# Kernel tuning notes

Hardware: AMD Instinct MI355X
Metric: run time of the kernel (lower is better)

Reference implementation:

```python
import jax, jax.numpy as jnp
import numpy as np

N, E = 50000, 640000          # nodes, edges
F_IN, HID, CLS = 128, 128, 64  # feature dims


def setup_inputs() -> dict:
    key = jax.random.key(0)
    ks = jax.random.split(key, 12)
    x = jax.random.normal(ks[0], (N, F_IN), dtype=jnp.float32)
    edge_index = jax.random.randint(ks[1], (2, E), 0, N, dtype=jnp.int32)
    s_in = 1.0 / np.sqrt(F_IN)
    s_h = 1.0 / np.sqrt(HID)
    return {
        "x": x,
        "edge_index": edge_index,
        "W0": jax.random.normal(ks[2], (F_IN, HID), jnp.float32) * s_in,
        "b0": jnp.zeros((HID,), jnp.float32),
        "W1": jax.random.normal(ks[3], (HID, HID), jnp.float32) * s_h,
        "b1": jnp.zeros((HID,), jnp.float32),
        "W2": jax.random.normal(ks[4], (HID, HID), jnp.float32) * s_h,
        "b2": jnp.zeros((HID,), jnp.float32),
        "W_lin": jax.random.normal(ks[5], (HID, CLS), jnp.float32) * s_h,
        "b_lin": jnp.zeros((CLS,), jnp.float32),
    }


def reference(x, edge_index, W0, b0, W1, b1, W2, b2, W_lin, b_lin):
    # GCNConv (PyG defaults): out = D^-1/2 (A + I) D^-1/2 (x @ W) + b
    row, col = edge_index[0], edge_index[1]  # source -> target
    # degree with self-loop (graph is fixed across layers, compute norms once)
    deg = jnp.zeros((N,), x.dtype).at[col].add(1.0) + 1.0
    dinv = jax.lax.rsqrt(deg)                 # deg >= 1, safe
    enorm = (dinv[row] * dinv[col])[:, None]  # [E,1] edge norm
    snorm = (dinv * dinv)[:, None]            # [N,1] self-loop norm

    def conv(h, W, b):
        h = h @ W                                             # [N,HID]
        agg = jnp.zeros_like(h).at[col].add(h[row] * enorm)   # neighbor agg
        return agg + h * snorm + b                            # + self loop + bias

    h = jax.nn.relu(conv(x, W0, b0))
    h = jax.nn.relu(conv(h, W1, b1))
    h = jax.nn.relu(conv(h, W2, b2))
    return h @ W_lin + b_lin
```

## Files before the change

kernel.cpp:

```cpp
#include <hip/hip_runtime.h>
#include <hip/hip_fp16.h>

#define N_NODES 50000
#define HID 128
#define CLS 64

#define NBINS 196
#define NBLK 256
#define LBUF_CAP 4096
#define WTOT 57344
#define GEMM0_BLOCKS 782
#define AROW 136

typedef __attribute__((ext_vector_type(8))) _Float16 f16x8;
typedef __attribute__((ext_vector_type(4))) float f32x4;

__device__ __forceinline__ float2 u2f2(unsigned int u) {
    union { unsigned int u; __half2 h; } c;
    c.u = u;
    return __half22float2(c.h);
}
__device__ __forceinline__ unsigned int f2u2(float a, float b) {
    union { unsigned int u; __half2 h; } c;
    c.h = __float22half2_rn(make_float2(a, b));
    return c.u;
}

__global__ __launch_bounds__(256) void hist_wsplit_kernel(
    const int* __restrict__ col, int* __restrict__ hist,
    const float* __restrict__ W0, const float* __restrict__ W1,
    const float* __restrict__ W2, const float* __restrict__ Wl,
    __half* __restrict__ o0h, __half* __restrict__ o0l,
    __half* __restrict__ o1h, __half* __restrict__ o1l,
    __half* __restrict__ o2h, __half* __restrict__ o2l,
    __half* __restrict__ o3h, __half* __restrict__ o3l,
    int E, int chunk) {
    int widx = blockIdx.x * 256 + threadIdx.x;
    if (widx < WTOT) {
        const float* W;
        __half *oh, *ol;
        int NCdim, local;
        if (widx < 16384)      { W = W0; oh = o0h; ol = o0l; NCdim = 128; local = widx; }
        else if (widx < 32768) { W = W1; oh = o1h; ol = o1l; NCdim = 128; local = widx - 16384; }
        else if (widx < 49152) { W = W2; oh = o2h; ol = o2l; NCdim = 128; local = widx - 32768; }
        else                   { W = Wl; oh = o3h; ol = o3l; NCdim = 64;  local = widx - 49152; }
        int nn = local >> 7;
        int k = local & 127;
        float v = W[(size_t)k * NCdim + nn];
        __half h = __float2half_rn(v);
        oh[local] = h;
        ol[local] = __float2half_rn(v - __half2float(h));
    }
    __shared__ int h[NBINS];
    for (int i = threadIdx.x; i < NBINS; i += 256) h[i] = 0;
    __syncthreads();
    int b = blockIdx.x;
    int beg = b * chunk;
    int end = min(E, beg + chunk);
    if (beg < end) {
        int vend = beg + ((end - beg) & ~3);
        for (int i = beg + threadIdx.x * 4; i < vend; i += 1024) {
            int4 c4 = *(const int4*)(col + i);
            atomicAdd(&h[c4.x >> 8], 1);
            atomicAdd(&h[c4.y >> 8], 1);
            atomicAdd(&h[c4.z >> 8], 1);
            atomicAdd(&h[c4.w >> 8], 1);
        }
        int i = vend + threadIdx.x;
        if (i < end) atomicAdd(&h[col[i] >> 8], 1);
    }
    __syncthreads();
    for (int i = threadIdx.x; i < NBINS; i += 256)
        hist[i * NBLK + b] = h[i];
}

__global__ __launch_bounds__(256) void scatter_kernel(
    const int* __restrict__ row, const int* __restrict__ col,
    const int* __restrict__ hist, int* __restrict__ binBase_g,
    int* __restrict__ sbuf_src, unsigned char* __restrict__ sbuf_c,
    int E, int chunk) {
    __shared__ int sTot[256];
    __shared__ int cur[NBINS];
    int b = blockIdx.x, t = threadIdx.x;
    int partial = 0, total = 0;
    if (t < NBINS) {
        const int4* r4 = (const int4*)(hist + t * NBLK);
        int nb4 = b >> 2, rem = b & 3;
        for (int j = 0; j < NBLK / 4; ++j) {
            int4 v = r4[j];
            int s = v.x + v.y + v.z + v.w;
            total += s;
            if (j < nb4) partial += s;
            else if (j == nb4) {
                if (rem > 0) partial += v.x;
                if (rem > 1) partial += v.y;
                if (rem > 2) partial += v.z;
            }
        }
    }
    sTot[t] = (t < NBINS) ? total : 0;
    __syncthreads();
#pragma unroll
    for (int off = 1; off < 256; off <<= 1) {
        int u = (t >= off) ? sTot[t - off] : 0;
        __syncthreads();
        sTot[t] += u;
        __syncthreads();
    }
    int myBase = sTot[t] - total;
    if (t < NBINS) cur[t] = myBase + partial;
    if (b == 0) {
        if (t < NBINS) binBase_g[t] = myBase;
        if (t == 0) binBase_g[NBINS] = E;
    }
    __syncthreads();
    int beg = b * chunk;
    int end = min(E, beg + chunk);
    if (beg >= end) return;
    int vend = beg + ((end - beg) & ~3);
    for (int i = beg + t * 4; i < vend; i += 1024) {
        int4 c4 = *(const int4*)(col + i);
        int4 r4 = *(const int4*)(row + i);
        int p;
        p = atomicAdd(&cur[c4.x >> 8], 1); sbuf_src[p] = r4.x; sbuf_c[p] = (unsigned char)(c4.x & 255);
        p = atomicAdd(&cur[c4.y >> 8], 1); sbuf_src[p] = r4.y; sbuf_c[p] = (unsigned char)(c4.y & 255);
        p = atomicAdd(&cur[c4.z >> 8], 1); sbuf_src[p] = r4.z; sbuf_c[p] = (unsigned char)(c4.z & 255);
        p = atomicAdd(&cur[c4.w >> 8], 1); sbuf_src[p] = r4.w; sbuf_c[p] = (unsigned char)(c4.w & 255);
    }
    int i = vend + t;
    if (i < end) {
        int c = col[i];
        int p = atomicAdd(&cur[c >> 8], 1);
        sbuf_src[p] = row[i];
        sbuf_c[p] = (unsigned char)(c & 255);
    }
}

__device__ __forceinline__ void gemm0_body(
    const float* __restrict__ x, const __half* __restrict__ Bh,
    const __half* __restrict__ Bl, __half* __restrict__ C, int M, int rowTile) {
    constexpr int NT = 8;
    int lane = threadIdx.x & 63;
    int m0 = rowTile << 4;
    if (m0 >= M) return;
    int mr = lane & 15;
    int kq = (lane >> 4) << 3;

    const float*  af = x + (size_t)(m0 + mr) * 128 + kq;
    const __half* bh = Bh + (size_t)mr * 128 + kq;
    const __half* bl = Bl + (size_t)mr * 128 + kq;

    f32x4 acc[NT];
#pragma unroll
    for (int t = 0; t < NT; ++t) acc[t] = (f32x4){0.f, 0.f, 0.f, 0.f};
#pragma unroll
    for (int kc = 0; kc < 128; kc += 32) {
        float4 lo = *(const float4*)(af + kc);
        float4 hi = *(const float4*)(af + kc + 4);
        f16x8 a;
        a[0] = (_Float16)lo.x; a[1] = (_Float16)lo.y;
        a[2] = (_Float16)lo.z; a[3] = (_Float16)lo.w;
        a[4] = (_Float16)hi.x; a[5] = (_Float16)hi.y;
        a[6] = (_Float16)hi.z; a[7] = (_Float16)hi.w;
#pragma unroll
        for (int t = 0; t < NT; ++t) {
            f16x8 wh = *(const f16x8*)(bh + (size_t)t * 16 * 128 + kc);
            f16x8 wl = *(const f16x8*)(bl + (size_t)t * 16 * 128 + kc);
            acc[t] = __builtin_amdgcn_mfma_f32_16x16x32_f16(a, wh, acc[t], 0, 0, 0);
            acc[t] = __builtin_amdgcn_mfma_f32_16x16x32_f16(a, wl, acc[t], 0, 0, 0);
        }
    }
    int r0 = m0 + ((lane >> 4) << 2);
    int cc = lane & 15;
#pragma unroll
    for (int t = 0; t < NT; ++t)
#pragma unroll
        for (int r = 0; r < 4; ++r)
            C[(size_t)(r0 + r) * 128 + t * 16 + cc] =
                __float2half_rn(acc[t][r]);
}

__global__ __launch_bounds__(256) void csrplace_gemm0_kernel(
    const int* __restrict__ binBase,
    const int* __restrict__ sbuf_src, const unsigned char* __restrict__ sbuf_c,
    float* __restrict__ dinv, int* __restrict__ row_ptr, int* __restrict__ csr_src,
    const float* __restrict__ x, const __half* __restrict__ W0h,
    const __half* __restrict__ W0l, __half* __restrict__ h2, int n, int E) {
    __shared__ int lcnt[256];
    __shared__ int lcur[256];
    __shared__ int ss[256];
    __shared__ int lbuf[LBUF_CAP];
    int b = blockIdx.x;
    if (b >= NBINS) {
        gemm0_body(x, W0h, W0l, h2, n, (b - NBINS) * 4 + (threadIdx.x >> 6));
        return;
    }
    int t = threadIdx.x;
    lcnt[t] = 0;
    __syncthreads();
    int beg = binBase[b], end = binBase[b + 1];
    for (int j = beg + t; j < end; j += 256)
        atomicAdd(&lcnt[sbuf_c[j]], 1);
    __syncthreads();
    int deg = lcnt[t];
    int node = b * 256 + t;
    if (node < n) dinv[node] = rsqrtf((float)deg + 1.0f);
    ss[t] = deg;
    __syncthreads();
#pragma unroll
    for (int off = 1; off < 256; off <<= 1) {
        int u = (t >= off) ? ss[t - off] : 0;
        __syncthreads();
        ss[t] += u;
        __syncthreads();
    }
    int excl = ss[t] - deg;
    lcur[t] = excl;
    int total = ss[255];
    if (node < n) row_ptr[node] = beg + excl;
    if (b == 0 && t == 0) row_ptr[n] = E;
    __syncthreads();
    for (int j = beg + t; j < end; j += 256) {
        int c = sbuf_c[j];
        int pos = atomicAdd(&lcur[c], 1);
        lbuf[pos] = sbuf_src[j];
    }
    __syncthreads();
    for (int j = t; j < total; j += 256) csr_src[beg + j] = lbuf[j];
}

__device__ __forceinline__ void gather_batch(
    const __half* __restrict__ h2, int msrc, float mw, int cnt,
    int hw, int foff, float4& acc) {
    int pairs = (cnt + 1) >> 1;
    int j = 0;
    for (; j + 4 <= pairs; j += 4) {
        int i0 = (j << 1) + hw,       i1 = ((j + 1) << 1) + hw;
        int i2 = ((j + 2) << 1) + hw, i3 = ((j + 3) << 1) + hw;
        int s0 = __shfl(msrc, i0), s1 = __shfl(msrc, i1);
        int s2 = __shfl(msrc, i2), s3 = __shfl(msrc, i3);
        float w0 = __shfl(mw, i0), w1 = __shfl(mw, i1);
        float w2 = __shfl(mw, i2), w3 = __shfl(mw, i3);
        uint2 r0 = *(const uint2*)(h2 + ((size_t)s0 << 7) + foff);
        uint2 r1 = *(const uint2*)(h2 + ((size_t)s1 << 7) + foff);
        uint2 r2 = *(const uint2*)(h2 + ((size_t)s2 << 7) + foff);
        uint2 r3 = *(const uint2*)(h2 + ((size_t)s3 << 7) + foff);
        float2 a0 = u2f2(r0.x), b0 = u2f2(r0.y);
        float2 a1 = u2f2(r1.x), b1 = u2f2(r1.y);
        float2 a2 = u2f2(r2.x), b2 = u2f2(r2.y);
        float2 a3 = u2f2(r3.x), b3 = u2f2(r3.y);
        acc.x = fmaf(a0.x, w0, acc.x); acc.y = fmaf(a0.y, w0, acc.y);
        acc.z = fmaf(b0.x, w0, acc.z); acc.w = fmaf(b0.y, w0, acc.w);
        acc.x = fmaf(a1.x, w1, acc.x); acc.y = fmaf(a1.y, w1, acc.y);
        acc.z = fmaf(b1.x, w1, acc.z); acc.w = fmaf(b1.y, w1, acc.w);
        acc.x = fmaf(a2.x, w2, acc.x); acc.y = fmaf(a2.y, w2, acc.y);
        acc.z = fmaf(b2.x, w2, acc.z); acc.w = fmaf(b2.y, w2, acc.w);
        acc.x = fmaf(a3.x, w3, acc.x); acc.y = fmaf(a3.y, w3, acc.y);
        acc.z = fmaf(b3.x, w3, acc.z); acc.w = fmaf(b3.y, w3, acc.w);
    }
    for (; j < pairs; ++j) {
        int i0 = (j << 1) + hw;
        int s0 = __shfl(msrc, i0);
        float w0 = __shfl(mw, i0);
        uint2 r0 = *(const uint2*)(h2 + ((size_t)s0 << 7) + foff);
        float2 a0 = u2f2(r0.x), b0 = u2f2(r0.y);
        acc.x = fmaf(a0.x, w0, acc.x); acc.y = fmaf(a0.y, w0, acc.y);
        acc.z = fmaf(b0.x, w0, acc.z); acc.w = fmaf(b0.y, w0, acc.w);
    }
}

template<int NC, bool HEAD>
__global__ __launch_bounds__(256) void agg_gemm_kernel(
    const __half* __restrict__ h2, const int* __restrict__ row_ptr,
    const int* __restrict__ csr_src, const float* __restrict__ dinv,
    const float* __restrict__ bias,
    const __half* __restrict__ Bh, const __half* __restrict__ Bl,
    const float* __restrict__ gbias, void* __restrict__ Cv, int n) {
    __shared__ __align__(16) __half Als[16][AROW];
    int wave = threadIdx.x >> 6;
    int lane = threadIdx.x & 63;
    int hw = lane >> 5;
    int foff = (lane & 31) << 2;
    int m0 = blockIdx.x << 4;
    int wid_base = m0 + wave * 4;

    int beg4[4], end4[4];
    float dv4[4];
#pragma unroll
    for (int k = 0; k < 4; ++k) {
        beg4[k] = row_ptr[wid_base + k];
        end4[k] = row_ptr[wid_base + k + 1];
        dv4[k] = dinv[wid_base + k];
    }
    int msrc4[4];
#pragma unroll
    for (int k = 0; k < 4; ++k) {
        int cnt = min(64, end4[k] - beg4[k]);
        msrc4[k] = 0;
        if (lane < cnt) msrc4[k] = csr_src[beg4[k] + lane];
    }
    float mw4[4];
#pragma unroll
    for (int k = 0; k < 4; ++k) {
        int cnt = min(64, end4[k] - beg4[k]);
        mw4[k] = 0.f;
        if (lane < cnt) mw4[k] = dinv[msrc4[k]] * dv4[k];
    }

#pragma unroll
    for (int k = 0; k < 4; ++k) {
        int wid = wid_base + k;
        float dv = dv4[k];
        float4 acc = make_float4(0.f, 0.f, 0.f, 0.f);
        int cnt0 = min(64, end4[k] - beg4[k]);
        gather_batch(h2, msrc4[k], mw4[k], cnt0, hw, foff, acc);
        for (int base = beg4[k] + 64; base < end4[k]; base += 64) {
            int cnt = min(64, end4[k] - base);
            int msrc = 0;
            float mw = 0.f;
            if (lane < cnt) {
                msrc = csr_src[base + lane];
                mw = dinv[msrc] * dv;
            }
            gather_batch(h2, msrc, mw, cnt, hw, foff, acc);
        }
        acc.x += __shfl_xor(acc.x, 32);
        acc.y += __shfl_xor(acc.y, 32);
        acc.z += __shfl_xor(acc.z, 32);
        acc.w += __shfl_xor(acc.w, 32);
        float sn = dv * dv;
        uint2 sr = *(const uint2*)(h2 + ((size_t)wid << 7) + foff);
        float2 s01 = u2f2(sr.x), s23 = u2f2(sr.y);
        float4 b4 = *(const float4*)(bias + foff);
        float o0 = fmaxf(fmaf(s01.x, sn, acc.x) + b4.x, 0.f);
        float o1 = fmaxf(fmaf(s01.y, sn, acc.y) + b4.y, 0.f);
        float o2 = fmaxf(fmaf(s23.x, sn, acc.z) + b4.z, 0.f);
        float o3 = fmaxf(fmaf(s23.y, sn, acc.w) + b4.w, 0.f);
        if (hw == 0) {
            int lr = wave * 4 + k;
            *(uint2*)&Als[lr][foff] = make_uint2(f2u2(o0, o1), f2u2(o2, o3));
        }
    }
    __syncthreads();

    constexpr int NT = NC / 16;
    constexpr int TPW = NT / 4;
    int mr = lane & 15;
    int kq = (lane >> 4) << 3;
    const __half* bh = Bh + (size_t)mr * 128 + kq;
    const __half* bl = Bl + (size_t)mr * 128 + kq;

    f32x4 acc[TPW];
#pragma unroll
    for (int t = 0; t < TPW; ++t) acc[t] = (f32x4){0.f, 0.f, 0.f, 0.f};
#pragma unroll
    for (int kc = 0; kc < 128; kc += 32) {
        f16x8 a = *(const f16x8*)&Als[mr][kq + kc];
#pragma unroll
        for (int t = 0; t < TPW; ++t) {
            int tile = wave * TPW + t;
            f16x8 wh = *(const f16x8*)(bh + (size_t)tile * 16 * 128 + kc);
            f16x8 wl = *(const f16x8*)(bl + (size_t)tile * 16 * 128 + kc);
            acc[t] = __builtin_amdgcn_mfma_f32_16x16x32_f16(a, wh, acc[t], 0, 0, 0);
            acc[t] = __builtin_amdgcn_mfma_f32_16x16x32_f16(a, wl, acc[t], 0, 0, 0);
        }
    }
    int r0 = m0 + ((lane >> 4) << 2);
    int cc = lane & 15;
#pragma unroll
    for (int t = 0; t < TPW; ++t) {
        int tile = wave * TPW + t;
        float bsv = HEAD ? gbias[tile * 16 + cc] : 0.f;
#pragma unroll
        for (int r = 0; r < 4; ++r) {
            if (r0 + r >= n) break;
            size_t idx = (size_t)(r0 + r) * NC + tile * 16 + cc;
            float val = acc[t][r] + bsv;
            if (HEAD)
                ((float*)Cv)[idx] = val;
            else
                ((__half*)Cv)[idx] = __float2half_rn(val);
        }
    }
}

extern "C" void kernel_launch(void* const* d_in, const int* in_sizes, int n_in,
                              void* d_out, int out_size, void* d_ws, size_t ws_size,
                              hipStream_t stream) {
    const float* x  = (const float*)d_in[0];
    const int* ei   = (const int*)d_in[1];
    const float* W0 = (const float*)d_in[2];
    const float* b0 = (const float*)d_in[3];
    const float* W1 = (const float*)d_in[4];
    const float* b1 = (const float*)d_in[5];
    const float* W2 = (const float*)d_in[6];
    const float* b2 = (const float*)d_in[7];
    const float* Wl = (const float*)d_in[8];
    const float* bl = (const float*)d_in[9];
    float* out = (float*)d_out;

    const int N = N_NODES;
    const int E = in_sizes[1] / 2;
    const int* row = ei;
    const int* col = ei + E;
    const int chunk = (((E + NBLK - 1) / NBLK) + 3) & ~3;

    char* ws = (char*)d_ws;
    auto alloc = [&](size_t bytes) {
        char* p = ws;
        ws += (bytes + 255) & ~(size_t)255;
        return p;
    };
    int*   hist    = (int*)alloc((size_t)NBINS * NBLK * 4);
    int*   binBase = (int*)alloc((size_t)(NBINS + 1) * 4);
    int*   sbuf_src= (int*)alloc((size_t)E * 4);
    unsigned char* sbuf_c = (unsigned char*)alloc((size_t)E);
    int*   row_ptr = (int*)alloc((size_t)(N + 1) * 4);
    float* dinv    = (float*)alloc((size_t)N * 4);
    int*   csr_src = (int*)alloc((size_t)E * 4);
    __half* h2a    = (__half*)alloc((size_t)N * HID * 2);
    __half* h2b    = (__half*)alloc((size_t)N * HID * 2);
    __half* Wt_h[4];
    __half* Wt_l[4];
    for (int i = 0; i < 3; ++i) {
        Wt_h[i] = (__half*)alloc((size_t)HID * HID * 2);
        Wt_l[i] = (__half*)alloc((size_t)HID * HID * 2);
    }
    Wt_h[3] = (__half*)alloc((size_t)CLS * HID * 2);
    Wt_l[3] = (__half*)alloc((size_t)CLS * HID * 2);

    hist_wsplit_kernel<<<NBLK, 256, 0, stream>>>(col, hist, W0, W1, W2, Wl,
        Wt_h[0], Wt_l[0], Wt_h[1], Wt_l[1], Wt_h[2], Wt_l[2], Wt_h[3], Wt_l[3], E, chunk);
    scatter_kernel<<<NBLK, 256, 0, stream>>>(row, col, hist, binBase, sbuf_src, sbuf_c, E, chunk);
    csrplace_gemm0_kernel<<<NBINS + GEMM0_BLOCKS, 256, 0, stream>>>(
        binBase, sbuf_src, sbuf_c, dinv, row_ptr, csr_src,
        x, Wt_h[0], Wt_l[0], h2a, N, E);

    const int fusedBlocks = (N + 15) / 16;

    agg_gemm_kernel<128, false><<<fusedBlocks, 256, 0, stream>>>(
        h2a, row_ptr, csr_src, dinv, b0, Wt_h[1], Wt_l[1], nullptr, h2b, N);
    agg_gemm_kernel<128, false><<<fusedBlocks, 256, 0, stream>>>(
        h2b, row_ptr, csr_src, dinv, b1, Wt_h[2], Wt_l[2], nullptr, h2a, N);
    agg_gemm_kernel<64, true><<<fusedBlocks, 256, 0, stream>>>(
        h2a, row_ptr, csr_src, dinv, b2, Wt_h[3], Wt_l[3], bl, out, N);
}
```

Measured before the change: 287.5 us.

## Interleave neighbor gathers across four rows with full-wave per-row feature split

Each wave now gathers for its four destination nodes together, looping to the maximum degree and issuing one edge per row per step. Each lane loads a half2 covering two features, so the whole 64-lane wave spans one 128-wide row instead of half-waves each handling four features and being reduced by a cross-half shuffle. This aims to keep more independent memory loads in flight and remove the reduction. Rows with fewer neighbors run masked, zero-weight iterations up to the group maximum, and each load is narrower. The row bound check in the GEMM store was also dropped, relying on N being a multiple of 16.

```diff
diff --git a/kernel.cpp b/kernel.cpp
--- a/kernel.cpp
+++ b/kernel.cpp
@@ -14,17 +14,6 @@
 
 typedef __attribute__((ext_vector_type(8))) _Float16 f16x8;
 typedef __attribute__((ext_vector_type(4))) float f32x4;
-
-__device__ __forceinline__ float2 u2f2(unsigned int u) {
-    union { unsigned int u; __half2 h; } c;
-    c.u = u;
-    return __half22float2(c.h);
-}
-__device__ __forceinline__ unsigned int f2u2(float a, float b) {
-    union { unsigned int u; __half2 h; } c;
-    c.h = __float22half2_rn(make_float2(a, b));
-    return c.u;
-}
 
 __global__ __launch_bounds__(256) void hist_wsplit_kernel(
     const int* __restrict__ col, int* __restrict__ hist,
@@ -229,46 +218,6 @@
     for (int j = t; j < total; j += 256) csr_src[beg + j] = lbuf[j];
 }
 
-__device__ __forceinline__ void gather_batch(
-    const __half* __restrict__ h2, int msrc, float mw, int cnt,
-    int hw, int foff, float4& acc) {
-    int pairs = (cnt + 1) >> 1;
-    int j = 0;
-    for (; j + 4 <= pairs; j += 4) {
-        int i0 = (j << 1) + hw,       i1 = ((j + 1) << 1) + hw;
-        int i2 = ((j + 2) << 1) + hw, i3 = ((j + 3) << 1) + hw;
-        int s0 = __shfl(msrc, i0), s1 = __shfl(msrc, i1);
-        int s2 = __shfl(msrc, i2), s3 = __shfl(msrc, i3);
-        float w0 = __shfl(mw, i0), w1 = __shfl(mw, i1);
-        float w2 = __shfl(mw, i2), w3 = __shfl(mw, i3);
-        uint2 r0 = *(const uint2*)(h2 + ((size_t)s0 << 7) + foff);
-        uint2 r1 = *(const uint2*)(h2 + ((size_t)s1 << 7) + foff);
-        uint2 r2 = *(const uint2*)(h2 + ((size_t)s2 << 7) + foff);
-        uint2 r3 = *(const uint2*)(h2 + ((size_t)s3 << 7) + foff);
-        float2 a0 = u2f2(r0.x), b0 = u2f2(r0.y);
-        float2 a1 = u2f2(r1.x), b1 = u2f2(r1.y);
-        float2 a2 = u2f2(r2.x), b2 = u2f2(r2.y);
-        float2 a3 = u2f2(r3.x), b3 = u2f2(r3.y);
-        acc.x = fmaf(a0.x, w0, acc.x); acc.y = fmaf(a0.y, w0, acc.y);
-        acc.z = fmaf(b0.x, w0, acc.z); acc.w = fmaf(b0.y, w0, acc.w);
-        acc.x = fmaf(a1.x, w1, acc.x); acc.y = fmaf(a1.y, w1, acc.y);
-        acc.z = fmaf(b1.x, w1, acc.z); acc.w = fmaf(b1.y, w1, acc.w);
-        acc.x = fmaf(a2.x, w2, acc.x); acc.y = fmaf(a2.y, w2, acc.y);
-        acc.z = fmaf(b2.x, w2, acc.z); acc.w = fmaf(b2.y, w2, acc.w);
-        acc.x = fmaf(a3.x, w3, acc.x); acc.y = fmaf(a3.y, w3, acc.y);
-        acc.z = fmaf(b3.x, w3, acc.z); acc.w = fmaf(b3.y, w3, acc.w);
-    }
-    for (; j < pairs; ++j) {
-        int i0 = (j << 1) + hw;
-        int s0 = __shfl(msrc, i0);
-        float w0 = __shfl(mw, i0);
-        uint2 r0 = *(const uint2*)(h2 + ((size_t)s0 << 7) + foff);
-        float2 a0 = u2f2(r0.x), b0 = u2f2(r0.y);
-        acc.x = fmaf(a0.x, w0, acc.x); acc.y = fmaf(a0.y, w0, acc.y);
-        acc.z = fmaf(b0.x, w0, acc.z); acc.w = fmaf(b0.y, w0, acc.w);
-    }
-}
-
 template<int NC, bool HEAD>
 __global__ __launch_bounds__(256) void agg_gemm_kernel(
     const __half* __restrict__ h2, const int* __restrict__ row_ptr,
@@ -279,67 +228,90 @@
     __shared__ __align__(16) __half Als[16][AROW];
     int wave = threadIdx.x >> 6;
     int lane = threadIdx.x & 63;
-    int hw = lane >> 5;
-    int foff = (lane & 31) << 2;
+    int loff = lane << 1;
     int m0 = blockIdx.x << 4;
     int wid_base = m0 + wave * 4;
 
-    int beg4[4], end4[4];
+    int beg4[4], end4[4], cnt4[4];
     float dv4[4];
 #pragma unroll
     for (int k = 0; k < 4; ++k) {
         beg4[k] = row_ptr[wid_base + k];
         end4[k] = row_ptr[wid_base + k + 1];
         dv4[k] = dinv[wid_base + k];
+        cnt4[k] = end4[k] - beg4[k];
     }
     int msrc4[4];
 #pragma unroll
     for (int k = 0; k < 4; ++k) {
-        int cnt = min(64, end4[k] - beg4[k]);
+        int c = min(64, cnt4[k]);
         msrc4[k] = 0;
-        if (lane < cnt) msrc4[k] = csr_src[beg4[k] + lane];
+        if (lane < c) msrc4[k] = csr_src[beg4[k] + lane];
     }
     float mw4[4];
 #pragma unroll
     for (int k = 0; k < 4; ++k) {
-        int cnt = min(64, end4[k] - beg4[k]);
+        int c = min(64, cnt4[k]);
         mw4[k] = 0.f;
-        if (lane < cnt) mw4[k] = dinv[msrc4[k]] * dv4[k];
-    }
-
+        if (lane < c) mw4[k] = dinv[msrc4[k]] * dv4[k];
+    }
+
+    float ax[4], ay[4];
+#pragma unroll
+    for (int k = 0; k < 4; ++k) { ax[k] = 0.f; ay[k] = 0.f; }
+
+    int maxc = max(max(cnt4[0], cnt4[1]), max(cnt4[2], cnt4[3]));
+    maxc = min(maxc, 64);
+    int j = 0;
+    for (; j + 2 <= maxc; j += 2) {
+#pragma unroll
+        for (int k = 0; k < 4; ++k) {
+            int sa = __shfl(msrc4[k], j);
+            int sb = __shfl(msrc4[k], j + 1);
+            float wa = __shfl(mw4[k], j);
+            float wb = __shfl(mw4[k], j + 1);
+            float2 va = __half22float2(*(const __half2*)(h2 + ((size_t)sa << 7) + loff));
+            float2 vb = __half22float2(*(const __half2*)(h2 + ((size_t)sb << 7) + loff));
+            ax[k] = fmaf(va.x, wa, ax[k]); ay[k] = fmaf(va.y, wa, ay[k]);
+            ax[k] = fmaf(vb.x, wb, ax[k]); ay[k] = fmaf(vb.y, wb, ay[k]);
+        }
+    }
+    if (j < maxc) {
+#pragma unroll
+        for (int k = 0; k < 4; ++k) {
+            int sa = __shfl(msrc4[k], j);
+            float wa = __shfl(mw4[k], j);
+            float2 va = __half22float2(*(const __half2*)(h2 + ((size_t)sa << 7) + loff));
+            ax[k] = fmaf(va.x, wa, ax[k]); ay[k] = fmaf(va.y, wa, ay[k]);
+        }
+    }
 #pragma unroll
     for (int k = 0; k < 4; ++k) {
-        int wid = wid_base + k;
-        float dv = dv4[k];
-        float4 acc = make_float4(0.f, 0.f, 0.f, 0.f);
-        int cnt0 = min(64, end4[k] - beg4[k]);
-        gather_batch(h2, msrc4[k], mw4[k], cnt0, hw, foff, acc);
         for (int base = beg4[k] + 64; base < end4[k]; base += 64) {
             int cnt = min(64, end4[k] - base);
             int msrc = 0;
             float mw = 0.f;
             if (lane < cnt) {
                 msrc = csr_src[base + lane];
-                mw = dinv[msrc] * dv;
+                mw = dinv[msrc] * dv4[k];
             }
-            gather_batch(h2, msrc, mw, cnt, hw, foff, acc);
-        }
-        acc.x += __shfl_xor(acc.x, 32);
-        acc.y += __shfl_xor(acc.y, 32);
-        acc.z += __shfl_xor(acc.z, 32);
-        acc.w += __shfl_xor(acc.w, 32);
-        float sn = dv * dv;
-        uint2 sr = *(const uint2*)(h2 + ((size_t)wid << 7) + foff);
-        float2 s01 = u2f2(sr.x), s23 = u2f2(sr.y);
-        float4 b4 = *(const float4*)(bias + foff);
-        float o0 = fmaxf(fmaf(s01.x, sn, acc.x) + b4.x, 0.f);
-        float o1 = fmaxf(fmaf(s01.y, sn, acc.y) + b4.y, 0.f);
-        float o2 = fmaxf(fmaf(s23.x, sn, acc.z) + b4.z, 0.f);
-        float o3 = fmaxf(fmaf(s23.y, sn, acc.w) + b4.w, 0.f);
-        if (hw == 0) {
-            int lr = wave * 4 + k;
-            *(uint2*)&Als[lr][foff] = make_uint2(f2u2(o0, o1), f2u2(o2, o3));
-        }
+            for (int jj = 0; jj < cnt; ++jj) {
+                int s = __shfl(msrc, jj);
+                float w = __shfl(mw, jj);
+                float2 v = __half22float2(*(const __half2*)(h2 + ((size_t)s << 7) + loff));
+                ax[k] = fmaf(v.x, w, ax[k]); ay[k] = fmaf(v.y, w, ay[k]);
+            }
+        }
+    }
+#pragma unroll
+    for (int k = 0; k < 4; ++k) {
+        int wid = wid_base + k;
+        float sn = dv4[k] * dv4[k];
+        float2 self = __half22float2(*(const __half2*)(h2 + ((size_t)wid << 7) + loff));
+        float2 b = *(const float2*)(bias + loff);
+        float ox = fmaxf(fmaf(self.x, sn, ax[k]) + b.x, 0.f);
+        float oy = fmaxf(fmaf(self.y, sn, ay[k]) + b.y, 0.f);
+        *(__half2*)&Als[wave * 4 + k][loff] = __float22half2_rn(make_float2(ox, oy));
     }
     __syncthreads();
 
@@ -373,7 +345,6 @@
         float bsv = HEAD ? gbias[tile * 16 + cc] : 0.f;
 #pragma unroll
         for (int r = 0; r < 4; ++r) {
-            if (r0 + r >= n) break;
             size_t idx = (size_t)(r0 + r) * NC + tile * 16 + cc;
             float val = acc[t][r] + bsv;
             if (HEAD)
```

Result: no change. 282.0 us (-1.9%).
